# Kernel tuning notes

Measured on AMD Instinct MI355X. Metric: run time of the kernel, lower is better.

## Reference

```python
import jax, jax.numpy as jnp
import numpy as np

H = 128  # hidden_dim


def setup_inputs() -> dict:
    key = jax.random.key(0)
    k1, k2, k3 = jax.random.split(key, 3)
    N = 1024
    return {
        "node_emb": jax.random.normal(k1, (N, H), dtype=jnp.float32),
        "W1": jax.random.normal(k2, (2 * H, H), dtype=jnp.float32) * 0.05,
        "b1": jnp.zeros((H,), dtype=jnp.float32),
        "W2": jax.random.normal(k3, (H, 1), dtype=jnp.float32) * 0.05,
        "b2": jnp.zeros((1,), dtype=jnp.float32),
    }


def reference(node_emb, W1, b1, W2, b2):
    # L2 normalize rows (torch F.normalize: x / max(||x||, eps))
    norm = jnp.sqrt(jnp.sum(node_emb * node_emb, axis=-1, keepdims=True))
    e = node_emb / jnp.maximum(norm, 1e-12)  # (N, H)
    # adj[i, j] = mlp(cat(e_i, e_j)); split W1 so we never materialize (N,N,2H)
    left = e @ W1[:H]    # (N, H) contribution of e_i
    right = e @ W1[H:]   # (N, H) contribution of e_j
    h = jax.nn.relu(left[:, None, :] + right[None, :, :] + b1)  # (N, N, H)
    logits = jnp.einsum("ijh,h->ij", h, W2[:, 0]) + b2[0]       # (N, N)
    return jax.nn.softmax(logits, axis=-1)
```

## Files before the change

kernel.cpp:

```cpp
#include <hip/hip_runtime.h>

#define H 128
#define N 1024

__global__ __launch_bounds__(512) void prep_kernel(
    const float* __restrict__ x, const float* __restrict__ W1,
    const float* __restrict__ b1, const float* __restrict__ W2,
    float* __restrict__ Lp, float* __restrict__ Rt, float* __restrict__ c)
{
    constexpr int PF = 8;
    __shared__ float e_s[4][H];
    __shared__ float cred[4][2];
    const int t = threadIdx.x;
    const int i0 = blockIdx.x * 4;

    if (t < 256) {
        const int row = t >> 6, lane = t & 63;
        const float2 v = *reinterpret_cast<const float2*>(&x[(i0 + row) * H + 2 * lane]);
        float s = v.x * v.x + v.y * v.y;
#pragma unroll
        for (int off = 32; off; off >>= 1) s += __shfl_xor(s, off);
        const float rn = 1.0f / fmaxf(sqrtf(s), 1e-12f);
        e_s[row][2 * lane]     = v.x * rn;
        e_s[row][2 * lane + 1] = v.y * rn;
    }
    __syncthreads();

    const int h = t & (H - 1);
    const int q = t >> 7;
    const int r0 = (q & 1) * 2;
    const float* Wb = W1 + (q >= 2 ? H * H : 0) + h;

    float acc0 = 0.f, acc1 = 0.f;
    float wbuf[PF];
#pragma unroll
    for (int p = 0; p < PF; ++p) wbuf[p] = Wb[p * H];

    for (int kb = 0; kb < H - PF; kb += PF) {
#pragma unroll
        for (int p = 0; p < PF; ++p) {
            const float w = wbuf[p];
            wbuf[p] = Wb[(kb + p + PF) * H];
            acc0 = fmaf(e_s[r0][kb + p],     w, acc0);
            acc1 = fmaf(e_s[r0 + 1][kb + p], w, acc1);
        }
    }
#pragma unroll
    for (int p = 0; p < PF; ++p) {
        const int k = H - PF + p;
        acc0 = fmaf(e_s[r0][k],     wbuf[p], acc0);
        acc1 = fmaf(e_s[r0 + 1][k], wbuf[p], acc1);
    }

    const float w2h = W2[h];
    if (q < 2) {
        const float bb = b1[h];
        Lp[(i0 + r0) * H + h]     = w2h * (acc0 + bb);
        Lp[(i0 + r0 + 1) * H + h] = w2h * (acc1 + bb);
    } else {
        const float v0 = w2h * acc0, v1 = w2h * acc1;
        Rt[h * N + (i0 + r0)]     = v0;
        Rt[h * N + (i0 + r0 + 1)] = v1;
        float s0 = v0, s1 = v1;
#pragma unroll
        for (int off = 32; off; off >>= 1) {
            s0 += __shfl_xor(s0, off);
            s1 += __shfl_xor(s1, off);
        }
        const int wv = t >> 6;
        if ((t & 63) == 0) { cred[wv - 4][0] = s0; cred[wv - 4][1] = s1; }
    }
    __syncthreads();
    if (t < 4) {
        const int r = t;
        c[i0 + r] = 0.5f * (cred[(r >> 1) * 2][r & 1] + cred[(r >> 1) * 2 + 1][r & 1]);
    }
}

__global__ __launch_bounds__(512) void adj_kernel(
    const float* __restrict__ Lp, const float* __restrict__ Rt,
    const float* __restrict__ W2, const float* __restrict__ c,
    float* __restrict__ out)
{
    constexpr int II = 4, PF = 8;
    __shared__ float LsT[H][4];
    __shared__ float sgn[H];
    __shared__ float red_m[II][8];
    __shared__ float red_s[II][8];

    const int t = threadIdx.x;
    const int lane = t & 63, wave = t >> 6;
    const int i0 = blockIdx.x * II;
    const int j0 = t * 2;

    if (t < H) {
        sgn[t] = (W2[t] >= 0.f) ? 0.5f : -0.5f;
        float4 lv;
        lv.x = Lp[(i0 + 0) * H + t];
        lv.y = Lp[(i0 + 1) * H + t];
        lv.z = Lp[(i0 + 2) * H + t];
        lv.w = Lp[(i0 + 3) * H + t];
        *reinterpret_cast<float4*>(&LsT[t][0]) = lv;
    }
    const float2 cj = *reinterpret_cast<const float2*>(&c[j0]);
    __syncthreads();

    float accx[II], accy[II];
#pragma unroll
    for (int ii = 0; ii < II; ++ii) { accx[ii] = cj.x; accy[ii] = cj.y; }

    float2 rbuf[PF];
#pragma unroll
    for (int p = 0; p < PF; ++p)
        rbuf[p] = *reinterpret_cast<const float2*>(&Rt[p * N + j0]);

    for (int hb = 0; hb < H - PF; hb += PF) {
#pragma unroll
        for (int p = 0; p < PF; ++p) {
            const int h = hb + p;
            const float2 r = rbuf[p];
            rbuf[p] = *reinterpret_cast<const float2*>(&Rt[(h + PF) * N + j0]);
            const float4 lv = *reinterpret_cast<const float4*>(&LsT[h][0]);
            const float s = sgn[h];
            const float* lp = &lv.x;
#pragma unroll
            for (int ii = 0; ii < II; ++ii) {
                accx[ii] = fmaf(s, fabsf(lp[ii] + r.x), accx[ii]);
                accy[ii] = fmaf(s, fabsf(lp[ii] + r.y), accy[ii]);
            }
        }
    }
#pragma unroll
    for (int p = 0; p < PF; ++p) {
        const int h = H - PF + p;
        const float2 r = rbuf[p];
        const float4 lv = *reinterpret_cast<const float4*>(&LsT[h][0]);
        const float s = sgn[h];
        const float* lp = &lv.x;
#pragma unroll
        for (int ii = 0; ii < II; ++ii) {
            accx[ii] = fmaf(s, fabsf(lp[ii] + r.x), accx[ii]);
            accy[ii] = fmaf(s, fabsf(lp[ii] + r.y), accy[ii]);
        }
    }

#pragma unroll
    for (int ii = 0; ii < II; ++ii) {
        float m = fmaxf(accx[ii], accy[ii]);
#pragma unroll
        for (int off = 32; off; off >>= 1) m = fmaxf(m, __shfl_xor(m, off));
        if (lane == 0) red_m[ii][wave] = m;
    }
    __syncthreads();

    float mm[II];
#pragma unroll
    for (int ii = 0; ii < II; ++ii) {
        float m = red_m[ii][0];
#pragma unroll
        for (int w = 1; w < 8; ++w) m = fmaxf(m, red_m[ii][w]);
        mm[ii] = m;
    }

#pragma unroll
    for (int ii = 0; ii < II; ++ii) {
        accx[ii] = expf(accx[ii] - mm[ii]);
        accy[ii] = expf(accy[ii] - mm[ii]);
        float s = accx[ii] + accy[ii];
#pragma unroll
        for (int off = 32; off; off >>= 1) s += __shfl_xor(s, off);
        if (lane == 0) red_s[ii][wave] = s;
    }
    __syncthreads();

#pragma unroll
    for (int ii = 0; ii < II; ++ii) {
        float s = red_s[ii][0];
#pragma unroll
        for (int w = 1; w < 8; ++w) s += red_s[ii][w];
        const float r = 1.0f / s;
        float2 o;
        o.x = accx[ii] * r;
        o.y = accy[ii] * r;
        *reinterpret_cast<float2*>(&out[(i0 + ii) * N + j0]) = o;
    }
}

extern "C" void kernel_launch(void* const* d_in, const int* in_sizes, int n_in,
                              void* d_out, int out_size, void* d_ws, size_t ws_size,
                              hipStream_t stream) {
    const float* x  = (const float*)d_in[0];
    const float* W1 = (const float*)d_in[1];
    const float* b1 = (const float*)d_in[2];
    const float* W2 = (const float*)d_in[3];
    float* out = (float*)d_out;

    float* Lp = (float*)d_ws;
    float* Rt = Lp + N * H;
    float* cc = Rt + H * N;

    prep_kernel<<<N / 4, 512, 0, stream>>>(x, W1, b1, W2, Lp, Rt, cc);
    adj_kernel<<<N / 4, 512, 0, stream>>>(Lp, Rt, W2, cc, out);
}
```

Measured before the change: 25.46 us.

## Partition hidden units by W2 sign to replace signed FMA with add/sub

The prep kernel ranks hidden units by the sign of W2 and writes the left and right projections into a permuted, sign-grouped slot layout. Each group is padded with zeros to a multiple of 8, and the bounds are published through a small meta buffer. The adj kernel then accumulates |L+R| with plain adds over positive slots and subtracts over negative slots, applying the 0.5 factor once at the end instead of multiplying by a per-h sign. This removes the per-h sign load and multiply and makes the left-operand staging a single float4 load per slot. In exchange it adds data-dependent loop bounds read from global memory, extra padding writes, and a larger workspace.

```diff
diff --git a/kernel.cpp b/kernel.cpp
--- a/kernel.cpp
+++ b/kernel.cpp
@@ -2,18 +2,31 @@
 
 #define H 128
 #define N 1024
+#define SLOTS 144
 
 __global__ __launch_bounds__(512) void prep_kernel(
     const float* __restrict__ x, const float* __restrict__ W1,
     const float* __restrict__ b1, const float* __restrict__ W2,
-    float* __restrict__ Lp, float* __restrict__ Rt, float* __restrict__ c)
+    float* __restrict__ LpS, float* __restrict__ Rt,
+    float* __restrict__ c, int* __restrict__ meta)
 {
     constexpr int PF = 8;
     __shared__ float e_s[4][H];
     __shared__ float cred[4][2];
+    __shared__ int   slot_s[H];
+    __shared__ int   cnt_s[2];
+    __shared__ int   meta_s[3];
     const int t = threadIdx.x;
     const int i0 = blockIdx.x * 4;
 
+    bool pos = false; int rank = 0;
+    if (t < H) {
+        const int lane = t & 63;
+        pos = (W2[t] >= 0.f);
+        const unsigned long long bal = __ballot(pos);
+        rank = __popcll(bal & ((1ull << lane) - 1ull));
+        if (lane == 0) cnt_s[t >> 6] = __popcll(bal);
+    }
     if (t < 256) {
         const int row = t >> 6, lane = t & 63;
         const float2 v = *reinterpret_cast<const float2*>(&x[(i0 + row) * H + 2 * lane]);
@@ -23,6 +36,23 @@
         const float rn = 1.0f / fmaxf(sqrtf(s), 1e-12f);
         e_s[row][2 * lane]     = v.x * rn;
         e_s[row][2 * lane + 1] = v.y * rn;
+    }
+    __syncthreads();
+
+    if (t < H) {
+        const int c0 = cnt_s[0];
+        const int P  = c0 + cnt_s[1];
+        const int P8 = (P + 7) & ~7;
+        const int lane = t & 63;
+        int slot;
+        if (pos) slot = (t < 64 ? 0 : c0) + rank;
+        else     slot = P8 + (t < 64 ? 0 : 64 - c0) + (lane - rank);
+        slot_s[t] = slot;
+        if (t == 0) {
+            meta_s[0] = P8;
+            meta_s[1] = P8 + ((H - P + 7) & ~7);
+            meta_s[2] = P;
+        }
     }
     __syncthreads();
 
@@ -53,14 +83,15 @@
     }
 
     const float w2h = W2[h];
+    const int slot = slot_s[h];
     if (q < 2) {
         const float bb = b1[h];
-        Lp[(i0 + r0) * H + h]     = w2h * (acc0 + bb);
-        Lp[(i0 + r0 + 1) * H + h] = w2h * (acc1 + bb);
+        LpS[slot * N + (i0 + r0)]     = w2h * (acc0 + bb);
+        LpS[slot * N + (i0 + r0 + 1)] = w2h * (acc1 + bb);
     } else {
         const float v0 = w2h * acc0, v1 = w2h * acc1;
-        Rt[h * N + (i0 + r0)]     = v0;
-        Rt[h * N + (i0 + r0 + 1)] = v1;
+        Rt[slot * N + (i0 + r0)]     = v0;
+        Rt[slot * N + (i0 + r0 + 1)] = v1;
         float s0 = v0, s1 = v1;
 #pragma unroll
         for (int off = 32; off; off >>= 1) {
@@ -71,20 +102,40 @@
         if ((t & 63) == 0) { cred[wv - 4][0] = s0; cred[wv - 4][1] = s1; }
     }
     __syncthreads();
-    if (t < 4) {
-        const int r = t;
-        c[i0 + r] = 0.5f * (cred[(r >> 1) * 2][r & 1] + cred[(r >> 1) * 2 + 1][r & 1]);
-    }
+
+    if (t < 4)
+        c[i0 + t] = cred[(t >> 1) * 2][t & 1] + cred[(t >> 1) * 2 + 1][t & 1];
+
+    {
+        const int P8m = meta_s[0], T8m = meta_s[1], Pm = meta_s[2];
+        const float4 z = {0.f, 0.f, 0.f, 0.f};
+        if (t >= 64 && t < 72) {
+            const int k = t - 64;
+            if (k < P8m - Pm) {
+                const int ps = Pm + k;
+                *reinterpret_cast<float4*>(&LpS[ps * N + i0]) = z;
+                *reinterpret_cast<float4*>(&Rt[ps * N + i0])  = z;
+            }
+        } else if (t >= 72 && t < 80) {
+            const int k = t - 72;
+            const int base2 = P8m + (H - Pm);
+            if (k < T8m - base2) {
+                const int ps = base2 + k;
+                *reinterpret_cast<float4*>(&LpS[ps * N + i0]) = z;
+                *reinterpret_cast<float4*>(&Rt[ps * N + i0])  = z;
+            }
+        }
+    }
+    if (blockIdx.x == 0 && t == 0) { meta[0] = meta_s[0]; meta[1] = meta_s[1]; }
 }
 
 __global__ __launch_bounds__(512) void adj_kernel(
-    const float* __restrict__ Lp, const float* __restrict__ Rt,
-    const float* __restrict__ W2, const float* __restrict__ c,
+    const float* __restrict__ LpS, const float* __restrict__ Rt,
+    const float* __restrict__ c, const int* __restrict__ meta,
     float* __restrict__ out)
 {
-    constexpr int II = 4, PF = 8;
-    __shared__ float LsT[H][4];
-    __shared__ float sgn[H];
+    constexpr int II = 4;
+    __shared__ float4 LsT[SLOTS];
     __shared__ float red_m[II][8];
     __shared__ float red_s[II][8];
 
@@ -93,15 +144,10 @@
     const int i0 = blockIdx.x * II;
     const int j0 = t * 2;
 
-    if (t < H) {
-        sgn[t] = (W2[t] >= 0.f) ? 0.5f : -0.5f;
-        float4 lv;
-        lv.x = Lp[(i0 + 0) * H + t];
-        lv.y = Lp[(i0 + 1) * H + t];
-        lv.z = Lp[(i0 + 2) * H + t];
-        lv.w = Lp[(i0 + 3) * H + t];
-        *reinterpret_cast<float4*>(&LsT[t][0]) = lv;
-    }
+    const int P8 = meta[0], T8 = meta[1];
+
+    if (t < T8)
+        LsT[t] = *reinterpret_cast<const float4*>(&LpS[t * N + i0]);
     const float2 cj = *reinterpret_cast<const float2*>(&c[j0]);
     __syncthreads();
 
@@ -109,40 +155,46 @@
 #pragma unroll
     for (int ii = 0; ii < II; ++ii) { accx[ii] = cj.x; accy[ii] = cj.y; }
 
-    float2 rbuf[PF];
-#pragma unroll
-    for (int p = 0; p < PF; ++p)
-        rbuf[p] = *reinterpret_cast<const float2*>(&Rt[p * N + j0]);
-
-    for (int hb = 0; hb < H - PF; hb += PF) {
-#pragma unroll
-        for (int p = 0; p < PF; ++p) {
-            const int h = hb + p;
+    const float* Rp = Rt + j0;
+    float2 rbuf[8];
+#pragma unroll
+    for (int p = 0; p < 8; ++p)
+        rbuf[p] = *reinterpret_cast<const float2*>(&Rp[p * N]);
+
+    int hb = 0;
+    for (; hb < P8; hb += 8) {
+#pragma unroll
+        for (int p = 0; p < 8; ++p) {
+            const int s = hb + p;
             const float2 r = rbuf[p];
-            rbuf[p] = *reinterpret_cast<const float2*>(&Rt[(h + PF) * N + j0]);
-            const float4 lv = *reinterpret_cast<const float4*>(&LsT[h][0]);
-            const float s = sgn[h];
+            rbuf[p] = *reinterpret_cast<const float2*>(&Rp[(s + 8) * N]);
+            const float4 lv = LsT[s];
             const float* lp = &lv.x;
 #pragma unroll
             for (int ii = 0; ii < II; ++ii) {
-                accx[ii] = fmaf(s, fabsf(lp[ii] + r.x), accx[ii]);
-                accy[ii] = fmaf(s, fabsf(lp[ii] + r.y), accy[ii]);
-            }
-        }
-    }
-#pragma unroll
-    for (int p = 0; p < PF; ++p) {
-        const int h = H - PF + p;
-        const float2 r = rbuf[p];
-        const float4 lv = *reinterpret_cast<const float4*>(&LsT[h][0]);
-        const float s = sgn[h];
-        const float* lp = &lv.x;
-#pragma unroll
-        for (int ii = 0; ii < II; ++ii) {
-            accx[ii] = fmaf(s, fabsf(lp[ii] + r.x), accx[ii]);
-            accy[ii] = fmaf(s, fabsf(lp[ii] + r.y), accy[ii]);
-        }
-    }
+                accx[ii] += fabsf(lp[ii] + r.x);
+                accy[ii] += fabsf(lp[ii] + r.y);
+            }
+        }
+    }
+    for (; hb < T8; hb += 8) {
+#pragma unroll
+        for (int p = 0; p < 8; ++p) {
+            const int s = hb + p;
+            const float2 r = rbuf[p];
+            rbuf[p] = *reinterpret_cast<const float2*>(&Rp[(s + 8) * N]);
+            const float4 lv = LsT[s];
+            const float* lp = &lv.x;
+#pragma unroll
+            for (int ii = 0; ii < II; ++ii) {
+                accx[ii] -= fabsf(lp[ii] + r.x);
+                accy[ii] -= fabsf(lp[ii] + r.y);
+            }
+        }
+    }
+
+#pragma unroll
+    for (int ii = 0; ii < II; ++ii) { accx[ii] *= 0.5f; accy[ii] *= 0.5f; }
 
 #pragma unroll
     for (int ii = 0; ii < II; ++ii) {
@@ -195,10 +247,12 @@
     const float* W2 = (const float*)d_in[3];
     float* out = (float*)d_out;
 
-    float* Lp = (float*)d_ws;
-    float* Rt = Lp + N * H;
-    float* cc = Rt + H * N;
-
-    prep_kernel<<<N / 4, 512, 0, stream>>>(x, W1, b1, W2, Lp, Rt, cc);
-    adj_kernel<<<N / 4, 512, 0, stream>>>(Lp, Rt, W2, cc, out);
+    float* wsf = (float*)d_ws;
+    float* LpS = wsf;
+    float* Rt  = LpS + SLOTS * N;
+    float* cc  = Rt + SLOTS * N;
+    int*   meta = (int*)(cc + N);
+
+    prep_kernel<<<N / 4, 512, 0, stream>>>(x, W1, b1, W2, LpS, Rt, cc, meta);
+    adj_kernel<<<N / 4, 512, 0, stream>>>(LpS, Rt, cc, meta, out);
 }
```

Measured after the change: 29.33 us. 1.15x slower.

## Store L transposed and stream it from global, dropping LDS staging in adj kernel

Applied to the files above, without the earlier changes.

The prep kernel now writes the left projection transposed (h-major, four rows packed as float4) through an LDS staging buffer, and scales by 0.5 instead of W2. The adj kernel loses its LDS staging of L, the sign table and the initial barrier. It prefetches the L float4 per h directly from global alongside R and multiplies by W2[h] in the inner loop. Buffers are padded to HPAD rows so the prefetch past h=127 stays in bounds. This removes a block-level sync and LDS reads in exchange for more global/cache loads and extra registers per thread.

```diff
diff --git a/kernel.cpp b/kernel.cpp
--- a/kernel.cpp
+++ b/kernel.cpp
@@ -2,15 +2,19 @@
 
 #define H 128
 #define N 1024
+#define HPAD 136
 
 __global__ __launch_bounds__(512) void prep_kernel(
     const float* __restrict__ x, const float* __restrict__ W1,
     const float* __restrict__ b1, const float* __restrict__ W2,
-    float* __restrict__ Lp, float* __restrict__ Rt, float* __restrict__ c)
+    float* __restrict__ At, float* __restrict__ Bt,
+    float* __restrict__ c)
 {
     constexpr int PF = 8;
     __shared__ float e_s[4][H];
     __shared__ float cred[4][2];
+    __shared__ float4 stageA[H];
+    __shared__ float4 stageB[H];
     const int t = threadIdx.x;
     const int i0 = blockIdx.x * 4;
 
@@ -52,16 +56,15 @@
         acc1 = fmaf(e_s[r0 + 1][k], wbuf[p], acc1);
     }
 
-    const float w2h = W2[h];
     if (q < 2) {
         const float bb = b1[h];
-        Lp[(i0 + r0) * H + h]     = w2h * (acc0 + bb);
-        Lp[(i0 + r0 + 1) * H + h] = w2h * (acc1 + bb);
+        float2 st; st.x = 0.5f * (acc0 + bb); st.y = 0.5f * (acc1 + bb);
+        *reinterpret_cast<float2*>(reinterpret_cast<float*>(&stageA[h]) + r0) = st;
     } else {
-        const float v0 = w2h * acc0, v1 = w2h * acc1;
-        Rt[h * N + (i0 + r0)]     = v0;
-        Rt[h * N + (i0 + r0 + 1)] = v1;
-        float s0 = v0, s1 = v1;
+        const float w2h = W2[h];
+        float2 st; st.x = 0.5f * acc0; st.y = 0.5f * acc1;
+        *reinterpret_cast<float2*>(reinterpret_cast<float*>(&stageB[h]) + r0) = st;
+        float s0 = w2h * acc0, s1 = w2h * acc1;
 #pragma unroll
         for (int off = 32; off; off >>= 1) {
             s0 += __shfl_xor(s0, off);
@@ -71,20 +74,21 @@
         if ((t & 63) == 0) { cred[wv - 4][0] = s0; cred[wv - 4][1] = s1; }
     }
     __syncthreads();
-    if (t < 4) {
-        const int r = t;
-        c[i0 + r] = 0.5f * (cred[(r >> 1) * 2][r & 1] + cred[(r >> 1) * 2 + 1][r & 1]);
-    }
+
+    if (t < 4)
+        c[i0 + t] = cred[(t >> 1) * 2][t & 1] + cred[(t >> 1) * 2 + 1][t & 1];
+    if (t < H)
+        *reinterpret_cast<float4*>(&At[t * N + i0]) = stageA[t];
+    else if (t >= 256 && t < 256 + H)
+        *reinterpret_cast<float4*>(&Bt[(t - 256) * N + i0]) = stageB[t - 256];
 }
 
 __global__ __launch_bounds__(512) void adj_kernel(
-    const float* __restrict__ Lp, const float* __restrict__ Rt,
+    const float* __restrict__ At, const float* __restrict__ Bt,
     const float* __restrict__ W2, const float* __restrict__ c,
     float* __restrict__ out)
 {
-    constexpr int II = 4, PF = 8;
-    __shared__ float LsT[H][4];
-    __shared__ float sgn[H];
+    constexpr int II = 4;
     __shared__ float red_m[II][8];
     __shared__ float red_s[II][8];
 
@@ -93,54 +97,36 @@
     const int i0 = blockIdx.x * II;
     const int j0 = t * 2;
 
-    if (t < H) {
-        sgn[t] = (W2[t] >= 0.f) ? 0.5f : -0.5f;
-        float4 lv;
-        lv.x = Lp[(i0 + 0) * H + t];
-        lv.y = Lp[(i0 + 1) * H + t];
-        lv.z = Lp[(i0 + 2) * H + t];
-        lv.w = Lp[(i0 + 3) * H + t];
-        *reinterpret_cast<float4*>(&LsT[t][0]) = lv;
-    }
     const float2 cj = *reinterpret_cast<const float2*>(&c[j0]);
-    __syncthreads();
-
     float accx[II], accy[II];
 #pragma unroll
-    for (int ii = 0; ii < II; ++ii) { accx[ii] = cj.x; accy[ii] = cj.y; }
+    for (int ii = 0; ii < II; ++ii) { accx[ii] = 0.5f * cj.x; accy[ii] = 0.5f * cj.y; }
 
-    float2 rbuf[PF];
+    const float* Bp = Bt + j0;
+    float2 rbuf[8];
+    float4 abuf[8];
 #pragma unroll
-    for (int p = 0; p < PF; ++p)
-        rbuf[p] = *reinterpret_cast<const float2*>(&Rt[p * N + j0]);
+    for (int p = 0; p < 8; ++p) {
+        rbuf[p] = *reinterpret_cast<const float2*>(&Bp[p * N]);
+        abuf[p] = *reinterpret_cast<const float4*>(&At[p * N + i0]);
+    }
 
-    for (int hb = 0; hb < H - PF; hb += PF) {
+#pragma unroll 1
+    for (int g = 0; g < H / 8; ++g) {
 #pragma unroll
-        for (int p = 0; p < PF; ++p) {
-            const int h = hb + p;
+        for (int p = 0; p < 8; ++p) {
+            const int s = 8 * g + p;
             const float2 r = rbuf[p];
-            rbuf[p] = *reinterpret_cast<const float2*>(&Rt[(h + PF) * N + j0]);
-            const float4 lv = *reinterpret_cast<const float4*>(&LsT[h][0]);
-            const float s = sgn[h];
-            const float* lp = &lv.x;
+            const float4 A = abuf[p];
+            rbuf[p] = *reinterpret_cast<const float2*>(&Bp[(s + 8) * N]);
+            abuf[p] = *reinterpret_cast<const float4*>(&At[(s + 8) * N + i0]);
+            const float w = W2[s];
+            const float* Ap = &A.x;
 #pragma unroll
             for (int ii = 0; ii < II; ++ii) {
-                accx[ii] = fmaf(s, fabsf(lp[ii] + r.x), accx[ii]);
-                accy[ii] = fmaf(s, fabsf(lp[ii] + r.y), accy[ii]);
+                accx[ii] = fmaf(w, fabsf(Ap[ii] + r.x), accx[ii]);
+                accy[ii] = fmaf(w, fabsf(Ap[ii] + r.y), accy[ii]);
             }
-        }
-    }
-#pragma unroll
-    for (int p = 0; p < PF; ++p) {
-        const int h = H - PF + p;
-        const float2 r = rbuf[p];
-        const float4 lv = *reinterpret_cast<const float4*>(&LsT[h][0]);
-        const float s = sgn[h];
-        const float* lp = &lv.x;
-#pragma unroll
-        for (int ii = 0; ii < II; ++ii) {
-            accx[ii] = fmaf(s, fabsf(lp[ii] + r.x), accx[ii]);
-            accy[ii] = fmaf(s, fabsf(lp[ii] + r.y), accy[ii]);
         }
     }
 
@@ -178,10 +164,10 @@
         float s = red_s[ii][0];
 #pragma unroll
         for (int w = 1; w < 8; ++w) s += red_s[ii][w];
-        const float r = 1.0f / s;
+        const float rcp = 1.0f / s;
         float2 o;
-        o.x = accx[ii] * r;
-        o.y = accy[ii] * r;
+        o.x = accx[ii] * rcp;
+        o.y = accy[ii] * rcp;
         *reinterpret_cast<float2*>(&out[(i0 + ii) * N + j0]) = o;
     }
 }
@@ -195,10 +181,11 @@
     const float* W2 = (const float*)d_in[3];
     float* out = (float*)d_out;
 
-    float* Lp = (float*)d_ws;
-    float* Rt = Lp + N * H;
-    float* cc = Rt + H * N;
+    float* wsf = (float*)d_ws;
+    float* At = wsf;
+    float* Bt = At + HPAD * N;
+    float* cc = Bt + HPAD * N;
 
-    prep_kernel<<<N / 4, 512, 0, stream>>>(x, W1, b1, W2, Lp, Rt, cc);
-    adj_kernel<<<N / 4, 512, 0, stream>>>(Lp, Rt, W2, cc, out);
+    prep_kernel<<<N / 4, 512, 0, stream>>>(x, W1, b1, W2, At, Bt, cc);
+    adj_kernel<<<N / 4, 512, 0, stream>>>(At, Bt, W2, cc, out);
 }
```

Result: slower. 30.34 us (+19.2%).

## Split adj rows across column tiles with a separate softmax combine kernel

Applied to the files above, without the earlier changes.

Each adj block now handles 16 rows by 256 columns instead of 4 rows by all 1024 columns, so each thread group of 128 threads reuses the same Rt column slice across 16 rows. Partial max and sum per column tile are written to workspace, and a new combine kernel rescales the unnormalized exponentials into the final softmax. This cuts the Rt global reads per output element. In exchange it adds a third launch and an extra read and write pass over the output matrix.

```diff
diff --git a/kernel.cpp b/kernel.cpp
--- a/kernel.cpp
+++ b/kernel.cpp
@@ -80,27 +80,35 @@
 __global__ __launch_bounds__(512) void adj_kernel(
     const float* __restrict__ Lp, const float* __restrict__ Rt,
     const float* __restrict__ W2, const float* __restrict__ c,
-    float* __restrict__ out)
+    float* __restrict__ out, float* __restrict__ m_arr,
+    float* __restrict__ s_arr)
 {
     constexpr int II = 4, PF = 8;
-    __shared__ float LsT[H][4];
+    __shared__ float LsT[H][16];
     __shared__ float sgn[H];
-    __shared__ float red_m[II][8];
-    __shared__ float red_s[II][8];
+    __shared__ float red_m[16][2];
+    __shared__ float red_s[16][2];
 
     const int t = threadIdx.x;
     const int lane = t & 63, wave = t >> 6;
-    const int i0 = blockIdx.x * II;
-    const int j0 = t * 2;
-
-    if (t < H) {
-        sgn[t] = (W2[t] >= 0.f) ? 0.5f : -0.5f;
+    const int bid = blockIdx.x;
+    const int js = bid & 3;
+    const int ib = bid >> 2;
+    const int i0 = ib * 16;
+    const int jbase = js * 256;
+    const int tg = t >> 7;
+    const int r0 = i0 + tg * 4;
+    const int j0 = jbase + (t & 127) * 2;
+
+    {
+        const int h = t & 127;
         float4 lv;
-        lv.x = Lp[(i0 + 0) * H + t];
-        lv.y = Lp[(i0 + 1) * H + t];
-        lv.z = Lp[(i0 + 2) * H + t];
-        lv.w = Lp[(i0 + 3) * H + t];
-        *reinterpret_cast<float4*>(&LsT[t][0]) = lv;
+        lv.x = Lp[(i0 + 4 * tg + 0) * H + h];
+        lv.y = Lp[(i0 + 4 * tg + 1) * H + h];
+        lv.z = Lp[(i0 + 4 * tg + 2) * H + h];
+        lv.w = Lp[(i0 + 4 * tg + 3) * H + h];
+        *reinterpret_cast<float4*>(&LsT[h][4 * tg]) = lv;
+        if (t < H) sgn[t] = (W2[t] >= 0.f) ? 0.5f : -0.5f;
     }
     const float2 cj = *reinterpret_cast<const float2*>(&c[j0]);
     __syncthreads();
@@ -120,7 +128,7 @@
             const int h = hb + p;
             const float2 r = rbuf[p];
             rbuf[p] = *reinterpret_cast<const float2*>(&Rt[(h + PF) * N + j0]);
-            const float4 lv = *reinterpret_cast<const float4*>(&LsT[h][0]);
+            const float4 lv = *reinterpret_cast<const float4*>(&LsT[h][4 * tg]);
             const float s = sgn[h];
             const float* lp = &lv.x;
 #pragma unroll
@@ -134,7 +142,7 @@
     for (int p = 0; p < PF; ++p) {
         const int h = H - PF + p;
         const float2 r = rbuf[p];
-        const float4 lv = *reinterpret_cast<const float4*>(&LsT[h][0]);
+        const float4 lv = *reinterpret_cast<const float4*>(&LsT[h][4 * tg]);
         const float s = sgn[h];
         const float* lp = &lv.x;
 #pragma unroll
@@ -149,18 +157,14 @@
         float m = fmaxf(accx[ii], accy[ii]);
 #pragma unroll
         for (int off = 32; off; off >>= 1) m = fmaxf(m, __shfl_xor(m, off));
-        if (lane == 0) red_m[ii][wave] = m;
+        if (lane == 0) red_m[4 * tg + ii][wave & 1] = m;
     }
     __syncthreads();
 
     float mm[II];
 #pragma unroll
-    for (int ii = 0; ii < II; ++ii) {
-        float m = red_m[ii][0];
-#pragma unroll
-        for (int w = 1; w < 8; ++w) m = fmaxf(m, red_m[ii][w]);
-        mm[ii] = m;
-    }
+    for (int ii = 0; ii < II; ++ii)
+        mm[ii] = fmaxf(red_m[4 * tg + ii][0], red_m[4 * tg + ii][1]);
 
 #pragma unroll
     for (int ii = 0; ii < II; ++ii) {
@@ -169,20 +173,51 @@
         float s = accx[ii] + accy[ii];
 #pragma unroll
         for (int off = 32; off; off >>= 1) s += __shfl_xor(s, off);
-        if (lane == 0) red_s[ii][wave] = s;
-    }
-    __syncthreads();
-
-#pragma unroll
-    for (int ii = 0; ii < II; ++ii) {
-        float s = red_s[ii][0];
-#pragma unroll
-        for (int w = 1; w < 8; ++w) s += red_s[ii][w];
-        const float r = 1.0f / s;
-        float2 o;
-        o.x = accx[ii] * r;
-        o.y = accy[ii] * r;
-        *reinterpret_cast<float2*>(&out[(i0 + ii) * N + j0]) = o;
+        if (lane == 0) red_s[4 * tg + ii][wave & 1] = s;
+        float2 o; o.x = accx[ii]; o.y = accy[ii];
+        *reinterpret_cast<float2*>(&out[(r0 + ii) * N + j0]) = o;
+    }
+    __syncthreads();
+
+    if ((t & 127) == 0) {
+#pragma unroll
+        for (int ii = 0; ii < II; ++ii) {
+            m_arr[(r0 + ii) * 4 + js] = mm[ii];
+            s_arr[(r0 + ii) * 4 + js] = red_s[4 * tg + ii][0] + red_s[4 * tg + ii][1];
+        }
+    }
+}
+
+__global__ __launch_bounds__(256) void comb_kernel(
+    float* __restrict__ out, const float* __restrict__ m_arr,
+    const float* __restrict__ s_arr)
+{
+    __shared__ float fs[4][4];
+    const int t = threadIdx.x;
+    const int i0 = blockIdx.x * 4;
+
+    if (t < 16) {
+        const int rr = t >> 2, js = t & 3;
+        const int i = i0 + rr;
+        const float m0 = m_arr[i * 4 + 0], m1 = m_arr[i * 4 + 1];
+        const float m2 = m_arr[i * 4 + 2], m3 = m_arr[i * 4 + 3];
+        const float M = fmaxf(fmaxf(m0, m1), fmaxf(m2, m3));
+        const float S = expf(m0 - M) * s_arr[i * 4 + 0]
+                      + expf(m1 - M) * s_arr[i * 4 + 1]
+                      + expf(m2 - M) * s_arr[i * 4 + 2]
+                      + expf(m3 - M) * s_arr[i * 4 + 3];
+        const float mj = (js == 0) ? m0 : (js == 1) ? m1 : (js == 2) ? m2 : m3;
+        fs[rr][js] = expf(mj - M) / S;
+    }
+    __syncthreads();
+
+    const int jsl = t >> 6;
+#pragma unroll
+    for (int rr = 0; rr < 4; ++rr) {
+        float4 v = *reinterpret_cast<const float4*>(&out[(i0 + rr) * N + 4 * t]);
+        const float f = fs[rr][jsl];
+        v.x *= f; v.y *= f; v.z *= f; v.w *= f;
+        *reinterpret_cast<float4*>(&out[(i0 + rr) * N + 4 * t]) = v;
     }
 }
 
@@ -198,7 +233,10 @@
     float* Lp = (float*)d_ws;
     float* Rt = Lp + N * H;
     float* cc = Rt + H * N;
+    float* m_arr = cc + N;
+    float* s_arr = m_arr + 4 * N;
 
     prep_kernel<<<N / 4, 512, 0, stream>>>(x, W1, b1, W2, Lp, Rt, cc);
-    adj_kernel<<<N / 4, 512, 0, stream>>>(Lp, Rt, W2, cc, out);
-}
+    adj_kernel<<<256, 512, 0, stream>>>(Lp, Rt, W2, cc, out, m_arr, s_arr);
+    comb_kernel<<<N / 4, 256, 0, stream>>>(out, m_arr, s_arr);
+}
```

Measured after the change: 30.06 us. 1.18x slower.
